# Performance work log

Hardware: AMD Instinct MI355X
Metric: run time of the kernel (lower is better)

The kernel has to match this reference:

```python
import jax, jax.numpy as jnp
import numpy as np

HIDDEN = 2048
NUM_HEADS = 32
NUM_KV_HEADS = 8
HEAD_DIM = HIDDEN // NUM_HEADS          # 64
Q_PER_KV = NUM_HEADS // NUM_KV_HEADS    # 4
KV_SIZE = HIDDEN * NUM_KV_HEADS // NUM_HEADS  # 512
BATCH, SEQ = 2, 2048


def setup_inputs() -> dict:
    key = jax.random.key(0)
    ks = jax.random.split(key, 10)
    s = 0.02
    return {
        "x": jax.random.normal(ks[0], (BATCH, SEQ, HIDDEN), jnp.float32),
        "attention_mask": jnp.zeros((BATCH, SEQ), jnp.float32),
        "Wq": jax.random.normal(ks[1], (HIDDEN, HIDDEN), jnp.float32) * s,
        "bq": jnp.zeros((HIDDEN,), jnp.float32),
        "Wk": jax.random.normal(ks[2], (HIDDEN, KV_SIZE), jnp.float32) * s,
        "bk": jnp.zeros((KV_SIZE,), jnp.float32),
        "Wv": jax.random.normal(ks[3], (HIDDEN, KV_SIZE), jnp.float32) * s,
        "bv": jnp.zeros((KV_SIZE,), jnp.float32),
        "Wo": jax.random.normal(ks[4], (HIDDEN, HIDDEN), jnp.float32) * s,
        "bo": jnp.zeros((HIDDEN,), jnp.float32),
    }


def reference(x, attention_mask, Wq, bq, Wk, bk, Wv, bv, Wo, bo):
    b, s, _ = x.shape
    q = x @ Wq + bq                                  # [b,s,H]
    k = x @ Wk + bk                                  # [b,s,kv_size]
    v = x @ Wv + bv
    # q -> [b, kv_heads, q_per_kv, s, head_dim]
    q = q.reshape(b, s, NUM_KV_HEADS, Q_PER_KV, HEAD_DIM).transpose(0, 2, 3, 1, 4)
    # k, v -> [b, kv_heads, s, head_dim]
    k = k.reshape(b, s, NUM_KV_HEADS, HEAD_DIM).transpose(0, 2, 1, 3)
    v = v.reshape(b, s, NUM_KV_HEADS, HEAD_DIM).transpose(0, 2, 1, 3)
    scale = 1.0 / jnp.sqrt(jnp.float32(HEAD_DIM))
    scores = jnp.einsum('bhqsd,bhkd->bhqsk', q, k) * scale   # [b,h,qpk,s,s]
    scores = scores + attention_mask.reshape(b, 1, 1, 1, s)
    attn = jax.nn.softmax(scores, axis=-1)
    out = jnp.einsum('bhqsk,bhkd->bhqsd', attn, v)           # [b,h,qpk,s,d]
    out = out.transpose(0, 3, 1, 2, 4).reshape(b, s, HIDDEN)
    return out @ Wo + bo
```

## Files before the change

kernel.cpp:

```cpp
#include <hip/hip_runtime.h>

typedef __attribute__((ext_vector_type(8))) short short8;
typedef __attribute__((ext_vector_type(4))) float floatx4;

#define B_ 2
#define S_ 2048
#define H_ 2048
#define LOG2E 1.44269504088896f

#define MFMA(a, b, c) __builtin_amdgcn_mfma_f32_16x16x32_bf16(a, b, c, 0, 0, 0)

__device__ __forceinline__ unsigned short f2bf(float f) {
    unsigned int x = __builtin_bit_cast(unsigned int, f);
    unsigned int r = x + 0x7FFFu + ((x >> 16) & 1u);
    return (unsigned short)(r >> 16);
}

__device__ __forceinline__ void gload_lds16(const unsigned short* g, unsigned short* l) {
    __builtin_amdgcn_global_load_lds(
        (const __attribute__((address_space(1))) void*)g,
        (__attribute__((address_space(3))) void*)l, 16, 0, 0);
}

__global__ __launch_bounds__(256) void conv_f2b(const float* __restrict__ in,
                                                unsigned short* __restrict__ out, int n4) {
    int i = blockIdx.x * 256 + threadIdx.x;
    if (i < n4) {
        float4 v = ((const float4*)in)[i];
        ushort4 o;
        o.x = f2bf(v.x); o.y = f2bf(v.y); o.z = f2bf(v.z); o.w = f2bf(v.w);
        ((ushort4*)out)[i] = o;
    }
}

__global__ __launch_bounds__(256) void tr_f2b(const float* __restrict__ in,
                                              unsigned short* __restrict__ out,
                                              int R, int C) {
    __shared__ unsigned short t[32][33];
    int c0 = blockIdx.x * 32, r0 = blockIdx.y * 32;
    int tx = threadIdx.x & 31, ty = threadIdx.x >> 5;
#pragma unroll
    for (int i = 0; i < 32; i += 8)
        t[ty + i][tx] = f2bf(in[(size_t)(r0 + ty + i) * C + c0 + tx]);
    __syncthreads();
#pragma unroll
    for (int i = 0; i < 32; i += 8)
        out[(size_t)(c0 + ty + i) * R + r0 + tx] = t[tx][ty + i];
}

__global__ __launch_bounds__(256) void tr_wqkv(const float* __restrict__ Wq,
                                               const float* __restrict__ Wk,
                                               const float* __restrict__ Wv,
                                               unsigned short* __restrict__ WqkvT) {
    __shared__ unsigned short t[32][33];
    int bx = blockIdx.x;
    const float* src; int C, c0, orow;
    if (bx < 64)      { src = Wq; C = 2048; c0 = bx * 32;        orow = bx * 32; }
    else if (bx < 80) { src = Wk; C = 512;  c0 = (bx - 64) * 32; orow = 2048 + (bx - 64) * 32; }
    else              { src = Wv; C = 512;  c0 = (bx - 80) * 32; orow = 2560 + (bx - 80) * 32; }
    int r0 = blockIdx.y * 32;
    int tx = threadIdx.x & 31, ty = threadIdx.x >> 5;
#pragma unroll
    for (int i = 0; i < 32; i += 8)
        t[ty + i][tx] = f2bf(src[(size_t)(r0 + ty + i) * C + c0 + tx]);
    __syncthreads();
#pragma unroll
    for (int i = 0; i < 32; i += 8)
        WqkvT[(size_t)(orow + ty + i) * 2048 + r0 + tx] = t[tx][ty + i];
}

__global__ __launch_bounds__(256) void tr_bf16(const unsigned short* __restrict__ in,
                                               unsigned short* __restrict__ out,
                                               int R, int C, int ipitch,
                                               size_t ibs, size_t obs) {
    __shared__ unsigned short t[32][33];
    in += (size_t)blockIdx.z * ibs; out += (size_t)blockIdx.z * obs;
    int c0 = blockIdx.x * 32, r0 = blockIdx.y * 32;
    int tx = threadIdx.x & 31, ty = threadIdx.x >> 5;
#pragma unroll
    for (int i = 0; i < 32; i += 8)
        t[ty + i][tx] = in[(size_t)(r0 + ty + i) * ipitch + c0 + tx];
    __syncthreads();
#pragma unroll
    for (int i = 0; i < 32; i += 8)
        out[(size_t)(c0 + ty + i) * R + r0 + tx] = t[tx][ty + i];
}

template <bool OUT_F32>
__global__ __launch_bounds__(256) void gemm_bt(const unsigned short* __restrict__ A,
                                               const unsigned short* __restrict__ Bt,
                                               const float* __restrict__ b0,
                                               const float* __restrict__ b1,
                                               const float* __restrict__ b2,
                                               int s1, int s2,
                                               void* __restrict__ Cv,
                                               int M, int N, int K) {
    __shared__ unsigned short As[128 * 64];
    __shared__ unsigned short Bs[128 * 64];
    const int t = threadIdx.x;
    const int lane = t & 63;
    const int wave = t >> 6;
    const int qlane = lane & 15;
    const int quad = lane >> 4;
    const int wm = (wave >> 1) * 64;
    const int wn = (wave & 1) * 64;
    const int bm = blockIdx.y * 128;
    const int bn = blockIdx.x * 128;
    const int srow = t >> 3;
    const int scc = (t & 7) * 8;
    const int gc8 = (((t & 7) ^ (2 * ((t >> 5) & 3))) * 8);
    const int rsw = 2 * (qlane >> 2);

    floatx4 acc[4][4] = {};

    for (int k0 = 0; k0 < K; k0 += 64) {
        __syncthreads();
#pragma unroll
        for (int r = 0; r < 4; ++r) {
            int row = r * 32 + srow;
            gload_lds16(A + (size_t)(bm + row) * K + k0 + gc8, &As[row * 64 + scc]);
        }
#pragma unroll
        for (int r = 0; r < 4; ++r) {
            int row = r * 32 + srow;
            gload_lds16(Bt + (size_t)(bn + row) * K + k0 + gc8, &Bs[row * 64 + scc]);
        }
        __syncthreads();
#pragma unroll
        for (int kk = 0; kk < 2; ++kk) {
            short8 a[4], b[4];
#pragma unroll
            for (int i = 0; i < 4; ++i)
                a[i] = *(const short8*)&As[(wm + i * 16 + qlane) * 64 + ((kk * 4 + quad) ^ rsw) * 8];
#pragma unroll
            for (int j = 0; j < 4; ++j)
                b[j] = *(const short8*)&Bs[(wn + j * 16 + qlane) * 64 + ((kk * 4 + quad) ^ rsw) * 8];
#pragma unroll
            for (int i = 0; i < 4; ++i)
#pragma unroll
                for (int j = 0; j < 4; ++j)
                    acc[i][j] = MFMA(a[i], b[j], acc[i][j]);
        }
    }
#pragma unroll
    for (int j = 0; j < 4; ++j) {
        int col = bn + wn + j * 16 + qlane;
        int cc = col; const float* bp = b0;
        if (col >= s2)      { bp = b2; cc = col - s2; }
        else if (col >= s1) { bp = b1; cc = col - s1; }
        float bvv = bp[cc];
#pragma unroll
        for (int i = 0; i < 4; ++i) {
            int row0 = bm + wm + i * 16 + quad * 4;
#pragma unroll
            for (int r = 0; r < 4; ++r) {
                float v = acc[i][j][r] + bvv;
                if (OUT_F32)
                    ((float*)Cv)[(size_t)(row0 + r) * N + col] = v;
                else
                    ((unsigned short*)Cv)[(size_t)(row0 + r) * N + col] = f2bf(v);
            }
        }
    }
}

__global__ __launch_bounds__(256, 4) void attn_kernel(const unsigned short* __restrict__ qkv,
                                                      const unsigned short* __restrict__ vtb,
                                                      const float* __restrict__ mask,
                                                      unsigned short* __restrict__ ob) {
    const int qt = blockIdx.x;
    const int head = blockIdx.y;
    const int b = blockIdx.z;
    const int kvh = head >> 2;
    const int qcol = head * 64;
    const int kcol = 2048 + kvh * 64;
    const int vch = kvh * 64;
    const int q0 = qt * 128;
    const int t = threadIdx.x;
    const int lane = t & 63;
    const int wave = t >> 6;
    const int qlane = lane & 15;
    const int quad = lane >> 4;
    const int wr = wave * 32;

    __shared__ unsigned short Ks[64 * 64];
    __shared__ unsigned short Vts[2][64 * 64];
    __shared__ unsigned short Ps[128 * 64];

    const int gc8 = (((t & 7) ^ (2 * ((t >> 5) & 3))) * 8);
    const int rsw = 2 * (qlane >> 2);
    const float scale2 = 0.125f * LOG2E;

    const unsigned short* vbase = vtb + (size_t)(b * 512 + vch) * S_;
    const float* mbase = mask + (size_t)b * S_;

    short8 aq[2][2];
#pragma unroll
    for (int mi = 0; mi < 2; ++mi)
#pragma unroll
        for (int kk = 0; kk < 2; ++kk)
            aq[mi][kk] = *(const short8*)(qkv +
                (size_t)(b * S_ + q0 + wr + mi * 16 + qlane) * 3072 + qcol + kk * 32 + quad * 8);

    {
        int row = t >> 3;
#pragma unroll
        for (int i = 0; i < 2; ++i) {
            int rr = row + 32 * i;
            gload_lds16(qkv + (size_t)(b * S_ + rr) * 3072 + kcol + gc8,
                        &Ks[(rr * 8 + (t & 7)) * 8]);
            gload_lds16(vbase + (size_t)rr * S_ + gc8,
                        &Vts[0][(rr * 8 + (t & 7)) * 8]);
        }
    }

    short8 ones;
    {
        short v = (qlane == 0) ? (short)0x3F80 : (short)0;
        ones = (short8){v, v, v, v, v, v, v, v};
    }

    floatx4 o[2][4] = {};
    floatx4 osum[2] = {};

    __syncthreads();

    for (int kt = 0; kt < 32; ++kt) {
        const int cur = kt & 1;

        if (kt < 31) {
            const int nxt = cur ^ 1;
            int kn = (kt + 1) * 64;
            int row = t >> 3;
#pragma unroll
            for (int i = 0; i < 2; ++i) {
                int rr = row + 32 * i;
                gload_lds16(vbase + (size_t)rr * S_ + kn + gc8,
                            &Vts[nxt][(rr * 8 + (t & 7)) * 8]);
            }
        }
        float m2[4];
#pragma unroll
        for (int j = 0; j < 4; ++j)
            m2[j] = mbase[kt * 64 + j * 16 + qlane] * LOG2E;

        floatx4 s[2][4] = {};
        __builtin_amdgcn_s_setprio(1);
#pragma unroll
        for (int j = 0; j < 4; ++j) {
            short8 bk0 = *(const short8*)&Ks[(j * 16 + qlane) * 64 + ((0 + quad) ^ rsw) * 8];
            short8 bk1 = *(const short8*)&Ks[(j * 16 + qlane) * 64 + ((4 + quad) ^ rsw) * 8];
#pragma unroll
            for (int mi = 0; mi < 2; ++mi) {
                s[mi][j] = MFMA(aq[mi][0], bk0, s[mi][j]);
                s[mi][j] = MFMA(aq[mi][1], bk1, s[mi][j]);
            }
        }
        __builtin_amdgcn_s_setprio(0);

#pragma unroll
        for (int mi = 0; mi < 2; ++mi)
#pragma unroll
            for (int j = 0; j < 4; ++j) {
                int ebase = (wr + mi * 16 + quad * 4) * 64 + 16 * (j ^ quad) + qlane;
#pragma unroll
                for (int r = 0; r < 4; ++r) {
                    float p = __builtin_amdgcn_exp2f(s[mi][j][r] * scale2 + m2[j]);
                    unsigned int u = __builtin_bit_cast(unsigned int, p) + 0x8000u;
                    Ps[ebase + r * 64] = (unsigned short)(u >> 16);
                }
            }

        __syncthreads();

        if (kt < 31) {
            int kn = (kt + 1) * 64;
            int row = t >> 3;
#pragma unroll
            for (int i = 0; i < 2; ++i) {
                int rr = row + 32 * i;
                gload_lds16(qkv + (size_t)(b * S_ + kn + rr) * 3072 + kcol + gc8,
                            &Ks[(rr * 8 + (t & 7)) * 8]);
            }
        }

        __builtin_amdgcn_s_setprio(1);
#pragma unroll
        for (int kk = 0; kk < 2; ++kk) {
            short8 ap[2];
#pragma unroll
            for (int mi = 0; mi < 2; ++mi)
                ap[mi] = *(const short8*)&Ps[(wr + mi * 16 + qlane) * 64 + ((kk * 4 + quad) ^ rsw) * 8];
#pragma unroll
            for (int j2 = 0; j2 < 4; ++j2) {
                short8 bv = *(const short8*)&Vts[cur][(j2 * 16 + qlane) * 64 + ((kk * 4 + quad) ^ rsw) * 8];
#pragma unroll
                for (int mi = 0; mi < 2; ++mi)
                    o[mi][j2] = MFMA(ap[mi], bv, o[mi][j2]);
            }
#pragma unroll
            for (int mi = 0; mi < 2; ++mi)
                osum[mi] = MFMA(ap[mi], ones, osum[mi]);
        }
        __builtin_amdgcn_s_setprio(0);

        __syncthreads();
    }

#pragma unroll
    for (int mi = 0; mi < 2; ++mi)
#pragma unroll
        for (int r = 0; r < 4; ++r) {
            float sm = __shfl(osum[mi][r], quad * 16, 64);
            float inv = 1.0f / sm;
            int row = q0 + wr + mi * 16 + quad * 4 + r;
#pragma unroll
            for (int j2 = 0; j2 < 4; ++j2)
                ob[(size_t)(b * S_ + row) * H_ + qcol + j2 * 16 + qlane] = f2bf(o[mi][j2][r] * inv);
        }
}

extern "C" void kernel_launch(void* const* d_in, const int* in_sizes, int n_in,
                              void* d_out, int out_size, void* d_ws, size_t ws_size,
                              hipStream_t stream) {
    const float* x    = (const float*)d_in[0];
    const float* mask = (const float*)d_in[1];
    const float* Wq   = (const float*)d_in[2];
    const float* bq   = (const float*)d_in[3];
    const float* Wk   = (const float*)d_in[4];
    const float* bk   = (const float*)d_in[5];
    const float* Wv   = (const float*)d_in[6];
    const float* bv   = (const float*)d_in[7];
    const float* Wo   = (const float*)d_in[8];
    const float* bo   = (const float*)d_in[9];
    float* out = (float*)d_out;

    unsigned short* ws = (unsigned short*)d_ws;
    unsigned short* x_bf   = ws;
    unsigned short* qkv    = x_bf + (size_t)4096 * 2048;
    unsigned short* vt_buf = qkv + (size_t)4096 * 3072;
    unsigned short* WqkvT  = vt_buf + (size_t)2 * 512 * 2048;
    unsigned short* WoT    = WqkvT;
    unsigned short* a_buf  = x_bf;

    const int BIG = 1 << 30;
    dim3 blk(256);
    conv_f2b<<<dim3(4096 * 2048 / 4 / 256), blk, 0, stream>>>(x, x_bf, 4096 * 2048 / 4);
    tr_wqkv<<<dim3(96, 64), blk, 0, stream>>>(Wq, Wk, Wv, WqkvT);
    gemm_bt<false><<<dim3(24, 32), blk, 0, stream>>>(x_bf, WqkvT, bq, bk, bv, 2048, 2560,
                                                     qkv, 4096, 3072, 2048);
    tr_f2b<<<dim3(64, 64), blk, 0, stream>>>(Wo, WoT, 2048, 2048);
    tr_bf16<<<dim3(16, 64, 2), blk, 0, stream>>>(qkv + 2560, vt_buf, 2048, 512, 3072,
                                                 (size_t)2048 * 3072, (size_t)512 * 2048);
    attn_kernel<<<dim3(16, 32, 2), blk, 0, stream>>>(qkv, vt_buf, mask, a_buf);
    gemm_bt<true><<<dim3(16, 32), blk, 0, stream>>>(a_buf, WoT, bo, bo, bo, BIG, BIG,
                                                    out, 4096, 2048, 2048);
}
```

Measured before the change: 350.9 us.

## Keep attention probabilities in registers by computing S transposed and permuting V

```diff
diff --git a/kernel.cpp b/kernel.cpp
--- a/kernel.cpp
+++ b/kernel.cpp
@@ -2,6 +2,7 @@
 
 typedef __attribute__((ext_vector_type(8))) short short8;
 typedef __attribute__((ext_vector_type(4))) float floatx4;
+typedef __attribute__((ext_vector_type(4))) unsigned int uintx4;
 
 #define B_ 2
 #define S_ 2048
@@ -69,10 +70,10 @@
         WqkvT[(size_t)(orow + ty + i) * 2048 + r0 + tx] = t[tx][ty + i];
 }
 
-__global__ __launch_bounds__(256) void tr_bf16(const unsigned short* __restrict__ in,
-                                               unsigned short* __restrict__ out,
-                                               int R, int C, int ipitch,
-                                               size_t ibs, size_t obs) {
+__global__ __launch_bounds__(256) void tr_vperm(const unsigned short* __restrict__ in,
+                                                unsigned short* __restrict__ out,
+                                                int R, int C, int ipitch,
+                                                size_t ibs, size_t obs) {
     __shared__ unsigned short t[32][33];
     in += (size_t)blockIdx.z * ibs; out += (size_t)blockIdx.z * obs;
     int c0 = blockIdx.x * 32, r0 = blockIdx.y * 32;
@@ -81,9 +82,13 @@
     for (int i = 0; i < 32; i += 8)
         t[ty + i][tx] = in[(size_t)(r0 + ty + i) * ipitch + c0 + tx];
     __syncthreads();
-#pragma unroll
-    for (int i = 0; i < 32; i += 8)
-        out[(size_t)(c0 + ty + i) * R + r0 + tx] = t[tx][ty + i];
+    int s = r0 + tx;
+    int sl = s & 63;
+    int j = sl >> 4, q = (sl >> 2) & 3, ii = sl & 3;
+    int sp = (s & ~63) + ((j >> 1) << 5) + (q << 3) + ((j & 1) << 2) + ii;
+#pragma unroll
+    for (int i = 0; i < 32; i += 8)
+        out[(size_t)(c0 + ty + i) * R + sp] = t[tx][ty + i];
 }
 
 template <bool OUT_F32>
@@ -185,7 +190,6 @@
 
     __shared__ unsigned short Ks[64 * 64];
     __shared__ unsigned short Vts[2][64 * 64];
-    __shared__ unsigned short Ps[128 * 64];
 
     const int gc8 = (((t & 7) ^ (2 * ((t >> 5) & 3))) * 8);
     const int rsw = 2 * (qlane >> 2);
@@ -239,37 +243,40 @@
                             &Vts[nxt][(rr * 8 + (t & 7)) * 8]);
             }
         }
-        float m2[4];
-#pragma unroll
-        for (int j = 0; j < 4; ++j)
-            m2[j] = mbase[kt * 64 + j * 16 + qlane] * LOG2E;
-
-        floatx4 s[2][4] = {};
-        __builtin_amdgcn_s_setprio(1);
-#pragma unroll
-        for (int j = 0; j < 4; ++j) {
-            short8 bk0 = *(const short8*)&Ks[(j * 16 + qlane) * 64 + ((0 + quad) ^ rsw) * 8];
-            short8 bk1 = *(const short8*)&Ks[(j * 16 + qlane) * 64 + ((4 + quad) ^ rsw) * 8];
-#pragma unroll
-            for (int mi = 0; mi < 2; ++mi) {
-                s[mi][j] = MFMA(aq[mi][0], bk0, s[mi][j]);
-                s[mi][j] = MFMA(aq[mi][1], bk1, s[mi][j]);
-            }
-        }
-        __builtin_amdgcn_s_setprio(0);
-
-#pragma unroll
-        for (int mi = 0; mi < 2; ++mi)
-#pragma unroll
-            for (int j = 0; j < 4; ++j) {
-                int ebase = (wr + mi * 16 + quad * 4) * 64 + 16 * (j ^ quad) + qlane;
-#pragma unroll
-                for (int r = 0; r < 4; ++r) {
-                    float p = __builtin_amdgcn_exp2f(s[mi][j][r] * scale2 + m2[j]);
-                    unsigned int u = __builtin_bit_cast(unsigned int, p) + 0x8000u;
-                    Ps[ebase + r * 64] = (unsigned short)(u >> 16);
+
+        unsigned int pk[2][4][2];
+#pragma unroll
+        for (int jj = 0; jj < 4; jj += 2) {
+            floatx4 st[2][2] = {};
+            __builtin_amdgcn_s_setprio(1);
+#pragma unroll
+            for (int dj = 0; dj < 2; ++dj) {
+                int j = jj + dj;
+                short8 bk0 = *(const short8*)&Ks[(j * 16 + qlane) * 64 + ((0 + quad) ^ rsw) * 8];
+                short8 bk1 = *(const short8*)&Ks[(j * 16 + qlane) * 64 + ((4 + quad) ^ rsw) * 8];
+#pragma unroll
+                for (int mi = 0; mi < 2; ++mi) {
+                    st[dj][mi] = MFMA(bk0, aq[mi][0], st[dj][mi]);
+                    st[dj][mi] = MFMA(bk1, aq[mi][1], st[dj][mi]);
                 }
             }
+            __builtin_amdgcn_s_setprio(0);
+#pragma unroll
+            for (int dj = 0; dj < 2; ++dj) {
+                int j = jj + dj;
+                floatx4 mv = *(const floatx4*)(mbase + kt * 64 + j * 16 + quad * 4);
+#pragma unroll
+                for (int mi = 0; mi < 2; ++mi)
+#pragma unroll
+                    for (int h = 0; h < 2; ++h) {
+                        float p0 = __builtin_amdgcn_exp2f(st[dj][mi][2 * h]     * scale2 + mv[2 * h]     * LOG2E);
+                        float p1 = __builtin_amdgcn_exp2f(st[dj][mi][2 * h + 1] * scale2 + mv[2 * h + 1] * LOG2E);
+                        unsigned int ua = __builtin_bit_cast(unsigned int, p0) + 0x8000u;
+                        unsigned int ub = __builtin_bit_cast(unsigned int, p1) + 0x8000u;
+                        pk[mi][j][h] = (ua >> 16) | (ub & 0xFFFF0000u);
+                    }
+            }
+        }
 
         __syncthreads();
 
@@ -289,8 +296,11 @@
         for (int kk = 0; kk < 2; ++kk) {
             short8 ap[2];
 #pragma unroll
-            for (int mi = 0; mi < 2; ++mi)
-                ap[mi] = *(const short8*)&Ps[(wr + mi * 16 + qlane) * 64 + ((kk * 4 + quad) ^ rsw) * 8];
+            for (int mi = 0; mi < 2; ++mi) {
+                uintx4 u = {pk[mi][2 * kk][0], pk[mi][2 * kk][1],
+                            pk[mi][2 * kk + 1][0], pk[mi][2 * kk + 1][1]};
+                ap[mi] = __builtin_bit_cast(short8, u);
+            }
 #pragma unroll
             for (int j2 = 0; j2 < 4; ++j2) {
                 short8 bv = *(const short8*)&Vts[cur][(j2 * 16 + qlane) * 64 + ((kk * 4 + quad) ^ rsw) * 8];
@@ -350,8 +360,8 @@
     gemm_bt<false><<<dim3(24, 32), blk, 0, stream>>>(x_bf, WqkvT, bq, bk, bv, 2048, 2560,
                                                      qkv, 4096, 3072, 2048);
     tr_f2b<<<dim3(64, 64), blk, 0, stream>>>(Wo, WoT, 2048, 2048);
-    tr_bf16<<<dim3(16, 64, 2), blk, 0, stream>>>(qkv + 2560, vt_buf, 2048, 512, 3072,
-                                                 (size_t)2048 * 3072, (size_t)512 * 2048);
+    tr_vperm<<<dim3(16, 64, 2), blk, 0, stream>>>(qkv + 2560, vt_buf, 2048, 512, 3072,
+                                                  (size_t)2048 * 3072, (size_t)512 * 2048);
     attn_kernel<<<dim3(16, 32, 2), blk, 0, stream>>>(qkv, vt_buf, mask, a_buf);
     gemm_bt<true><<<dim3(16, 32), blk, 0, stream>>>(a_buf, WoT, bo, bo, bo, BIG, BIG,
                                                     out, 4096, 2048, 2048);
```

Result: no change. 347.6 us (-0.9%).
